# Performance work log

Measured on AMD Instinct MI355X. Metric: run time of the kernel, lower is better.

## Reference

```python
import jax, jax.numpy as jnp
import numpy as np

INF = 1e30  # sentinel for 'unreached' cost
MAX_ITERS = 512


def setup_inputs() -> dict:
    key = jax.random.key(0)
    img = jax.random.uniform(key, (3, 2048, 2048), dtype=jnp.float32)
    return {"img": img}


def _sobel_mag(gray):
    # gray: [H,W] -> gradient magnitude [H,W] (the 'processing_filter')
    kx = jnp.array([[-1.0, 0.0, 1.0], [-2.0, 0.0, 2.0], [-1.0, 0.0, 1.0]], gray.dtype)
    k = jnp.stack([kx, kx.T])[:, None]  # [2,1,3,3]
    g = jax.lax.conv_general_dilated(gray[None, None], k, (1, 1), 'SAME')[0]  # [2,H,W]
    return jnp.sqrt(g[0] ** 2 + g[1] ** 2)


def _neighbor_min(c):
    # min over 4-connected neighbors, INF padding at borders
    big_r = jnp.full((1, c.shape[1]), INF, c.dtype)
    big_c = jnp.full((c.shape[0], 1), INF, c.dtype)
    n = jnp.concatenate([big_r, c[:-1]], 0)
    s = jnp.concatenate([c[1:], big_r], 0)
    w = jnp.concatenate([big_c, c[:, :-1]], 1)
    e = jnp.concatenate([c[:, 1:], big_c], 1)
    return jnp.minimum(jnp.minimum(n, s), jnp.minimum(w, e))


def _relax(cost, img):
    # minimax-path (flood-level) relaxation: cost[p] = min(cost[p], max(min_nbr_cost, img[p]))
    return jnp.minimum(cost, jnp.maximum(_neighbor_min(cost), img))


def _watershed2(img, markers):
    # marker-based watershed on topography `img` with labels {1,2}.
    # Label of p = argmin over seed sets of the minimax path cost (flooding level),
    # which matches skimage.segmentation.watershed region assignment (4-connectivity).
    c1 = jnp.where(markers == 1, img, jnp.float32(INF))
    c2 = jnp.where(markers == 2, img, jnp.float32(INF))

    def cond(st):
        _, _, i, ch = st
        return jnp.logical_and(ch, i < MAX_ITERS)

    def body(st):
        c1, c2, i, _ = st
        n1 = _relax(c1, img)
        n2 = _relax(c2, img)
        ch = jnp.logical_or(jnp.any(n1 < c1), jnp.any(n2 < c2))
        return n1, n2, i + 1, ch

    c1, c2, _, _ = jax.lax.while_loop(cond, body, (c1, c2, jnp.int32(0), jnp.bool_(True)))
    return jnp.where(c2 < c1, jnp.float32(2.0), jnp.float32(1.0))


def _forward(img):
    gray = jnp.einsum('chw,c->hw', img, jnp.array([0.2989, 0.587, 0.114], img.dtype))
    filter_res = _sobel_mag(gray)  # [H,W]
    q_hi = jnp.quantile(filter_res, 0.9925)
    q_lo = jnp.quantile(filter_res, 0.9825)
    # torch sets 2 first, then 1, so pixels satisfying both end up as 1
    markers = jnp.where(filter_res <= q_lo, 1, jnp.where(filter_res >= q_hi, 2, 0))
    labels = _watershed2(gray, markers)[None]  # [1,H,W], values in {1,2}
    labels = labels - labels.min()
    return labels / labels.max()


def reference(img):
    return _forward(img)
```

## Files before the change

### kernel.cpp

```cpp
#include <hip/hip_runtime.h>
#include <hip/hip_cooperative_groups.h>

#define HH 2048
#define WW 2048
#define NPX (HH*WW)
#define INFV 1e30f
#define TS 128
#define NT 16
#define NTL 256
#define CY 32

namespace cg = cooperative_groups;

__device__ __forceinline__ void BARL(){
  __builtin_amdgcn_sched_barrier(0);
  asm volatile("s_waitcnt lgkmcnt(0)" ::: "memory");
  __builtin_amdgcn_s_barrier();
  __builtin_amdgcn_sched_barrier(0);
}

__device__ __forceinline__ float sobel_at(const float* __restrict__ g, int y, int x){
  float a00,a01,a02,a10,a12,a20,a21,a22;
  if (y>0 && y<HH-1 && x>0 && x<WW-1){
    const float* p = g + (size_t)(y-1)*WW + x;
    a00=p[-1]; a01=p[0]; a02=p[1];
    p += WW;   a10=p[-1];          a12=p[1];
    p += WW;   a20=p[-1]; a21=p[0]; a22=p[1];
  } else {
    auto at=[&](int yy,int xx)->float{
      return (yy<0||yy>=HH||xx<0||xx>=WW)?0.0f:g[(size_t)yy*WW+xx];
    };
    a00=at(y-1,x-1); a01=at(y-1,x); a02=at(y-1,x+1);
    a10=at(y,  x-1);                a12=at(y,  x+1);
    a20=at(y+1,x-1); a21=at(y+1,x); a22=at(y+1,x+1);
  }
  float gx = __fadd_rn(__fadd_rn(__fsub_rn(a02,a00), __fmul_rn(2.0f,__fsub_rn(a12,a10))), __fsub_rn(a22,a20));
  float gy = __fadd_rn(__fadd_rn(__fsub_rn(a20,a00), __fmul_rn(2.0f,__fsub_rn(a21,a01))), __fsub_rn(a22,a02));
  return sqrtf(__fadd_rn(__fmul_rn(gx,gx),__fmul_rn(gy,gy)));
}

__global__ void gray_kernel(const float* __restrict__ img, float* __restrict__ gray){
  const float* R=img; const float* G=img+NPX; const float* B=img+2*(size_t)NPX;
  for (int i=blockIdx.x*blockDim.x+threadIdx.x; i<NPX; i+=gridDim.x*blockDim.x){
    gray[i] = __fadd_rn(__fadd_rn(__fmul_rn(0.2989f,R[i]),__fmul_rn(0.587f,G[i])),__fmul_rn(0.114f,B[i]));
  }
}

__global__ void sobel_hist1(const float* __restrict__ gray, float* __restrict__ fr,
                            unsigned* __restrict__ hist){
  __shared__ unsigned h[4*2048];
  for (int i=threadIdx.x;i<4*2048;i+=blockDim.x) h[i]=0;
  __syncthreads();
  const int rep=(threadIdx.x&3)*2048;
  for (int i=blockIdx.x*blockDim.x+threadIdx.x; i<NPX; i+=gridDim.x*blockDim.x){
    int y=i>>11, x=i&(WW-1);
    float f=sobel_at(gray,y,x);
    fr[i]=f;
    unsigned key=__float_as_uint(f);
    atomicAdd(&h[rep+(key>>21)],1u);
  }
  __syncthreads();
  for (int i=threadIdx.x;i<2048;i+=blockDim.x){
    unsigned s=h[i]+h[i+2048]+h[i+4096]+h[i+6144];
    if (s) atomicAdd(&hist[i],s);
  }
}

__global__ void hist_l2(const float* __restrict__ fr, const unsigned* __restrict__ sel1,
                        unsigned* __restrict__ hist2){
  __shared__ unsigned h[4*2048];
  __shared__ unsigned sb[4];
  if (threadIdx.x<4) sb[threadIdx.x]=sel1[threadIdx.x];
  for (int i=threadIdx.x;i<4*2048;i+=blockDim.x) h[i]=0;
  __syncthreads();
  for (int i=blockIdx.x*blockDim.x+threadIdx.x; i<NPX; i+=gridDim.x*blockDim.x){
    unsigned key=__float_as_uint(fr[i]);
    unsigned b=key>>21, sub=(key>>10)&0x7FFu;
    #pragma unroll
    for (int k=0;k<4;++k) if (b==sb[k]) atomicAdd(&h[k*2048+sub],1u);
  }
  __syncthreads();
  for (int i=threadIdx.x;i<4*2048;i+=blockDim.x){ unsigned s=h[i]; if (s) atomicAdd(&hist2[i],s); }
}

__global__ void hist_l3(const float* __restrict__ fr, const unsigned* __restrict__ sel1,
                        const unsigned* __restrict__ sel2, unsigned* __restrict__ hist3){
  __shared__ unsigned h[4*1024];
  __shared__ unsigned pf[4];
  if (threadIdx.x<4) pf[threadIdx.x]=(sel1[threadIdx.x]<<11)|sel2[threadIdx.x];
  for (int i=threadIdx.x;i<4*1024;i+=blockDim.x) h[i]=0;
  __syncthreads();
  for (int i=blockIdx.x*blockDim.x+threadIdx.x; i<NPX; i+=gridDim.x*blockDim.x){
    unsigned key=__float_as_uint(fr[i]);
    unsigned p22=key>>10, sub=key&0x3FFu;
    #pragma unroll
    for (int k=0;k<4;++k) if (p22==pf[k]) atomicAdd(&h[k*1024+sub],1u);
  }
  __syncthreads();
  for (int i=threadIdx.x;i<4*1024;i+=blockDim.x){ unsigned s=h[i]; if (s) atomicAdd(&hist3[i],s); }
}

__global__ void scan_l1(const unsigned* __restrict__ hist, unsigned* __restrict__ sel1,
                        unsigned* __restrict__ rem1){
  __shared__ unsigned part[1024];
  const int t=threadIdx.x;
  unsigned a=hist[2*t], b=hist[2*t+1];
  part[t]=a+b; __syncthreads();
  for (int off=1;off<1024;off<<=1){
    unsigned add=(t>=off)?part[t-off]:0u; __syncthreads();
    part[t]+=add; __syncthreads();
  }
  unsigned before=(t>0)?part[t-1]:0u;
  const unsigned R[4]={4120902u,4120903u,4162845u,4162846u};
  unsigned cum=before;
  #pragma unroll
  for (int i=0;i<4;++i) if (R[i]>=cum && R[i]<cum+a){ sel1[i]=2*t;   rem1[i]=R[i]-cum; }
  cum+=a;
  #pragma unroll
  for (int i=0;i<4;++i) if (R[i]>=cum && R[i]<cum+b){ sel1[i]=2*t+1; rem1[i]=R[i]-cum; }
}

__global__ void scan_l2(const unsigned* __restrict__ hist2, const unsigned* __restrict__ rem1,
                        unsigned* __restrict__ sel2, unsigned* __restrict__ rem2){
  __shared__ unsigned part[1024];
  const int t=threadIdx.x;
  for (int i=0;i<4;++i){
    const unsigned* hh=hist2+i*2048;
    unsigned a=hh[2*t], b=hh[2*t+1];
    part[t]=a+b; __syncthreads();
    for (int off=1;off<1024;off<<=1){
      unsigned add=(t>=off)?part[t-off]:0u; __syncthreads();
      part[t]+=add; __syncthreads();
    }
    unsigned before=(t>0)?part[t-1]:0u;
    unsigned r=rem1[i], cum=before;
    if (r>=cum && r<cum+a){ sel2[i]=2*t;   rem2[i]=r-cum; }
    cum+=a;
    if (r>=cum && r<cum+b){ sel2[i]=2*t+1; rem2[i]=r-cum; }
    __syncthreads();
  }
}

__global__ void scan_l3(const unsigned* __restrict__ hist3, const unsigned* __restrict__ sel1,
                        const unsigned* __restrict__ sel2, const unsigned* __restrict__ rem2,
                        float* __restrict__ scal){
  __shared__ unsigned part[1024];
  __shared__ float vals[4];
  const int t=threadIdx.x;
  for (int i=0;i<4;++i){
    unsigned c=hist3[i*1024+t];
    part[t]=c; __syncthreads();
    for (int off=1;off<1024;off<<=1){
      unsigned add=(t>=off)?part[t-off]:0u; __syncthreads();
      part[t]+=add; __syncthreads();
    }
    unsigned before=(t>0)?part[t-1]:0u;
    unsigned r=rem2[i];
    if (r>=before && r<before+c){
      unsigned key=(sel1[i]<<21)|(sel2[i]<<10)|(unsigned)t;
      vals[i]=__uint_as_float(key);
    }
    __syncthreads();
  }
  if (t==0){
    scal[0]=__fadd_rn(__fmul_rn(vals[0],0.25f),__fmul_rn(vals[1],0.75f));
    scal[1]=__fadd_rn(__fmul_rn(vals[2],0.25f),__fmul_rn(vals[3],0.75f));
  }
}


#define HSCAN_LR(va,vb,gA,gB,hl) do{ \
  float ql_=gA[j], qh_=va[j]; \
  qh_=fminf(vb[j],fmaxf(gB[j],qh_)); ql_=fmaxf(gB[j],ql_); \
  _Pragma("unroll") \
  for (int d_=1;d_<64;d_<<=1){ \
    float pl_=__shfl_up(ql_,(unsigned)d_), ph_=__shfl_up(qh_,(unsigned)d_); \
    if (c>=d_){ qh_=fminf(qh_,fmaxf(ql_,ph_)); ql_=fmaxf(ql_,pl_); } \
  } \
  float E_=fminf(qh_,fmaxf(ql_,(hl))); \
  float In_=__shfl_up(E_,1u); if(c==0) In_=(hl); \
  float na_=fminf(va[j],fmaxf(gA[j],In_)); if(na_<va[j]){va[j]=na_;ch=true;} \
  float nb_=fminf(vb[j],fmaxf(gB[j],na_)); if(nb_<vb[j]){vb[j]=nb_;ch=true;} \
}while(0)

#define HSCAN_RL(va,vb,gA,gB,hr) do{ \
  float ql_=gB[j], qh_=vb[j]; \
  qh_=fminf(va[j],fmaxf(gA[j],qh_)); ql_=fmaxf(gA[j],ql_); \
  _Pragma("unroll") \
  for (int d_=1;d_<64;d_<<=1){ \
    float pl_=__shfl_down(ql_,(unsigned)d_), ph_=__shfl_down(qh_,(unsigned)d_); \
    if (c+d_<64){ qh_=fminf(qh_,fmaxf(ql_,ph_)); ql_=fmaxf(ql_,pl_); } \
  } \
  float E_=fminf(qh_,fmaxf(ql_,(hr))); \
  float In_=__shfl_down(E_,1u); if(c==63) In_=(hr); \
  float nb_=fminf(vb[j],fmaxf(gB[j],In_)); if(nb_<vb[j]){vb[j]=nb_;ch=true;} \
  float na_=fminf(va[j],fmaxf(gA[j],nb_)); if(na_<va[j]){va[j]=na_;ch=true;} \
}while(0)

#define VCOMP_DN(va,gA,Larr,Harr,XX) { float ql_=gA[0], qh_=va[0]; \
  _Pragma("unroll") for (int jj_=1;jj_<8;++jj_){ qh_=fminf(va[jj_],fmaxf(gA[jj_],qh_)); ql_=fmaxf(gA[jj_],ql_);} \
  Larr[w][XX]=ql_; Harr[w][XX]=qh_; }

#define VCOMP_UP(va,gA,Larr,Harr,XX) { float ql_=gA[7], qh_=va[7]; \
  _Pragma("unroll") for (int jj_=6;jj_>=0;--jj_){ qh_=fminf(va[jj_],fmaxf(gA[jj_],qh_)); ql_=fmaxf(gA[jj_],ql_);} \
  Larr[w][XX]=ql_; Harr[w][XX]=qh_; }

#define VAPPLY_DN(va,gA,Larr,XX) { float In_=Larr[w][XX]; \
  _Pragma("unroll") for (int jj_=0;jj_<8;++jj_){ float nv_=fminf(va[jj_],fmaxf(In_,gA[jj_])); if(nv_<va[jj_]){va[jj_]=nv_;ch=true;} In_=nv_; } }

#define VAPPLY_UP(va,gA,Larr,XX) { float In_=Larr[w][XX]; \
  _Pragma("unroll") for (int jj_=7;jj_>=0;--jj_){ float nv_=fminf(va[jj_],fmaxf(In_,gA[jj_])); if(nv_<va[jj_]){va[jj_]=nv_;ch=true;} In_=nv_; } }

#define CHAIN_DN(Harr,Larr,HT) { float E=HALO[HT][x]; \
  _Pragma("unroll") for (int b_=0;b_<16;++b_){ float I=E; E=fminf(Harr[b_][x],fmaxf(Larr[b_][x],I)); Larr[b_][x]=I; } }

#define CHAIN_UP(Harr,Larr,HB) { float E=HALO[HB][x]; \
  _Pragma("unroll") for (int b_=15;b_>=0;--b_){ float I=E; E=fminf(Harr[b_][x],fmaxf(Larr[b_][x],I)); Larr[b_][x]=I; } }

#define CHAINC_DN(Harr,Larr,Earr,HT,ECHV) { \
  float E=HALO[HT][x]; unsigned m_=0; \
  _Pragma("unroll") for (int b_=0;b_<16;++b_){ \
    float I_=E; E=fminf(Harr[b_][x],fmaxf(Larr[b_][x],I_)); \
    if (__any(I_!=Earr[b_][x])) m_|=(1u<<b_); \
    Earr[b_][x]=I_; } \
  if (c==0 && m_) atomicOr(&ECHV,(int)m_); }

#define CHAINC_UP(Harr,Larr,Earr,HB,ECHV) { \
  float E=HALO[HB][x]; unsigned m_=0; \
  _Pragma("unroll") for (int b_=15;b_>=0;--b_){ \
    float I_=E; E=fminf(Harr[b_][x],fmaxf(Larr[b_][x],I_)); \
    if (__any(I_!=Earr[b_][x])) m_|=(1u<<b_); \
    Earr[b_][x]=I_; } \
  if (c==0 && m_) atomicOr(&ECHV,(int)m_); }

#define HFIELD(va,vb,IHL,IHR) do{ \
  _Pragma("unroll") \
  for (int j=0;j<8;++j){ \
    const int r_=(w<<3)|j; \
    const float hl=HALO[IHL][r_], hr=HALO[IHR][r_]; \
    { float la_=__shfl_up(vb[j],1u); if(c==0) la_=hl; \
      bool p_=__any((fminf(va[j],fmaxf(la_,ga[j]))<va[j])||(fminf(vb[j],fmaxf(va[j],gb[j]))<vb[j])); \
      if (p_){ HSCAN_LR(va,vb,ga,gb,hl); } } \
    { float ra_=__shfl_down(va[j],1u); if(c==63) ra_=hr; \
      bool p_=__any((fminf(vb[j],fmaxf(ra_,gb[j]))<vb[j])||(fminf(va[j],fmaxf(vb[j],ga[j]))<va[j])); \
      if (p_){ HSCAN_RL(va,vb,ga,gb,hr); } } \
  } \
}while(0)

#define ASTORE(p,v) __hip_atomic_store((p),(v),__ATOMIC_RELAXED,__HIP_MEMORY_SCOPE_AGENT)
#define ALOAD(p)    __hip_atomic_load((p),__ATOMIC_RELAXED,__HIP_MEMORY_SCOPE_AGENT)

__global__ void __launch_bounds__(1024,4)
tile_solve(float* __restrict__ c1g, float* __restrict__ cg,
           const float* __restrict__ grayg, const float* __restrict__ scal)
{
  __shared__ float DNL1[16][128], DNH1[16][128], DNL2[16][128], DNH2[16][128];
  __shared__ float UPL1[16][128], UPH1[16][128], UPL2[16][128], UPH2[16][128];
  __shared__ float HALO[8][128];
  __shared__ int VN1[2],HN1[2],VN2[2],HN2[2];
  const int tid=threadIdx.x, w=tid>>6, c=tid&63;
  const int oty=blockIdx.x>>5, otx=blockIdx.x&31;
  const int wy0=oty*64-32, wx0=otx*64-32, x0=c<<1;
  const float qlo=scal[0], qhi=scal[1];
  HALO[tid>>7][tid&127]=INFV;
  if (tid==0){ VN1[0]=1;HN1[0]=1;VN2[0]=1;HN2[0]=1;
               VN1[1]=0;HN1[1]=0;VN2[1]=0;HN2[1]=0; }
  float v1a[8],v1b[8],v2a[8],v2b[8],ga[8],gb[8];
  const int gx=wx0+x0;
  #pragma unroll
  for (int j=0;j<8;++j){
    const int gy=wy0+(w<<3)+j;
    const bool rok=(gy>=0)&&(gy<HH);
    const bool aok=rok&&(gx>=0)&&(gx<WW), bok=rok&&(gx+1>=0)&&(gx+1<WW);
    float gA=INFV,gB=INFV,fA=0.0f,fB=0.0f;
    if (aok){ gA=grayg[(size_t)gy*WW+gx];   fA=sobel_at(grayg,gy,gx); }
    if (bok){ gB=grayg[(size_t)gy*WW+gx+1]; fB=sobel_at(grayg,gy,gx+1); }
    ga[j]=gA; gb[j]=gB;
    if (aok){ bool m1=(fA<=qlo); bool m2=(!m1)&&(fA>=qhi);
              v1a[j]=m1?gA:INFV; v2a[j]=(m1|m2)?gA:INFV; }
    else    { v1a[j]=INFV; v2a[j]=INFV; }
    if (bok){ bool m1=(fB<=qlo); bool m2=(!m1)&&(fB>=qhi);
              v1b[j]=m1?gB:INFV; v2b[j]=(m1|m2)?gB:INFV; }
    else    { v1b[j]=INFV; v2b[j]=INFV; }
  }
  __syncthreads();
  for (int cyc=0; cyc<24; ++cyc){
    const int cur=cyc&1, nxt=cur^1;
    const int vn1=VN1[cur], hn1=HN1[cur], vn2=VN2[cur], hn2=HN2[cur];
    if (!(vn1|hn1|vn2|hn2)) break;
    if (vn1){
      VCOMP_DN(v1a,ga,DNL1,DNH1,x0) VCOMP_DN(v1b,gb,DNL1,DNH1,x0+1)
      VCOMP_UP(v1a,ga,UPL1,UPH1,x0) VCOMP_UP(v1b,gb,UPL1,UPH1,x0+1)
    }
    if (vn2){
      VCOMP_DN(v2a,ga,DNL2,DNH2,x0) VCOMP_DN(v2b,gb,DNL2,DNH2,x0+1)
      VCOMP_UP(v2a,ga,UPL2,UPH2,x0) VCOMP_UP(v2b,gb,UPL2,UPH2,x0+1)
    }
    __syncthreads();
    if (w<8){
      const int x=((w&1)<<6)|c;
      const bool go=(w>>2)?(vn2!=0):(vn1!=0);
      if (go){
        switch(w>>1){
          case 0: CHAIN_DN(DNH1,DNL1,0) break;
          case 1: CHAIN_UP(UPH1,UPL1,2) break;
          case 2: CHAIN_DN(DNH2,DNL2,1) break;
          default:CHAIN_UP(UPH2,UPL2,3) break;
        }
      }
    }
    __syncthreads();
    if (vn1){ bool ch=false;
      VAPPLY_DN(v1a,ga,DNL1,x0) VAPPLY_DN(v1b,gb,DNL1,x0+1)
      VAPPLY_UP(v1a,ga,UPL1,x0) VAPPLY_UP(v1b,gb,UPL1,x0+1)
      if (ch) HN1[nxt]=1;
    }
    if (hn1){ bool ch=false;
      HFIELD(v1a,v1b,4,6);
      if (ch) VN1[nxt]=1;
    }
    if (vn2){ bool ch=false;
      VAPPLY_DN(v2a,ga,DNL2,x0) VAPPLY_DN(v2b,gb,DNL2,x0+1)
      VAPPLY_UP(v2a,ga,UPL2,x0) VAPPLY_UP(v2b,gb,UPL2,x0+1)
      if (ch) HN2[nxt]=1;
    }
    if (hn2){ bool ch=false;
      HFIELD(v2a,v2b,5,7);
      if (ch) VN2[nxt]=1;
    }
    if (tid==0){ VN1[cur]=0; HN1[cur]=0; VN2[cur]=0; HN2[cur]=0; }
    __syncthreads();
  }
  if (w>=4 && w<12 && c>=16 && c<48){
    #pragma unroll
    for (int j=0;j<8;++j){
      const int gy=wy0+(w<<3)+j;
      const size_t b=(size_t)gy*WW+gx;
      float2 o1; o1.x=v1a[j]; o1.y=v1b[j];
      float2 o2; o2.x=v2a[j]; o2.y=v2b[j];
      *(float2*)(c1g+b)=o1;
      *(float2*)(cg +b)=o2;
    }
  }
}

#define CYCLE(HV,CUR,NXT) do{ \
  if (hsrc){ \
    if (HV < HALO[harr][hx]){ \
      HALO[harr][hx]=HV; \
      if (harr<4){ if (harr&1) VN2[NXT]=1; else VN1[NXT]=1; } \
      else       { if (harr&1) HN2[NXT]=1; else HN1[NXT]=1; } \
    } \
    HV=ALOAD(hsrc); \
  } \
  const int vn1=VN1[CUR], hn1=HN1[CUR], vn2=VN2[CUR], hn2=HN2[CUR]; \
  const unsigned vd1=(unsigned)VD1s, vd2=(unsigned)VD2s; \
  if (!(vn1|hn1|vn2|hn2|(int)(vd1|vd2))){ \
    BARL(); \
  } else { \
     \
    if ((vd1>>w)&1){ \
      VCOMP_DN(v1a,ga,DNL1,DNH1,x0) VCOMP_DN(v1b,gb,DNL1,DNH1,x0+1) \
      VCOMP_UP(v1a,ga,UPL1,UPH1,x0) VCOMP_UP(v1b,gb,UPL1,UPH1,x0+1) \
    } \
    if ((vd2>>w)&1){ \
      VCOMP_DN(v2a,ga,DNL2,DNH2,x0) VCOMP_DN(v2b,gb,DNL2,DNH2,x0+1) \
      VCOMP_UP(v2a,ga,UPL2,UPH2,x0) VCOMP_UP(v2b,gb,UPL2,UPH2,x0+1) \
    } \
    if (tid==0){ ECH1s=0; ECH2s=0; } \
    BARL(); \
     \
    if (w<8){ \
      const int x=((w&1)<<6)|c; \
      switch(w>>1){ \
        case 0: if (vn1|(int)vd1) CHAINC_DN(DNH1,DNL1,EDN1,0,ECH1s) break; \
        case 1: if (vn1|(int)vd1) CHAINC_UP(UPH1,UPL1,EUP1,2,ECH1s) break; \
        case 2: if (vn2|(int)vd2) CHAINC_DN(DNH2,DNL2,EDN2,1,ECH2s) break; \
        default:if (vn2|(int)vd2) CHAINC_UP(UPH2,UPL2,EUP2,3,ECH2s) break; \
      } \
    } \
    if (tid==0){ VD1s=0; VD2s=0; } \
    BARL(); \
     \
    const unsigned am1=((unsigned)ECH1s)|vd1, am2=((unsigned)ECH2s)|vd2; \
    bool pf1=false, pf2=false; \
    { bool ch=false; \
      if ((am1>>w)&1){ \
        VAPPLY_DN(v1a,ga,EDN1,x0) VAPPLY_DN(v1b,gb,EDN1,x0+1) \
        VAPPLY_UP(v1a,ga,EUP1,x0) VAPPLY_UP(v1b,gb,EUP1,x0+1) \
      } \
      bool vch=__any(ch); \
      ch=false; \
      if (hn1){ HFIELD(v1a,v1b,4,6); } \
      bool hch=__any(ch); \
      if ((vch|hch) && c==0) atomicOr(&VD1s,1<<w); \
      if (vch) HN1[NXT]=1; \
      pf1 = vch|hch; \
    } \
    { bool ch=false; \
      if ((am2>>w)&1){ \
        VAPPLY_DN(v2a,ga,EDN2,x0) VAPPLY_DN(v2b,gb,EDN2,x0+1) \
        VAPPLY_UP(v2a,ga,EUP2,x0) VAPPLY_UP(v2b,gb,EUP2,x0+1) \
      } \
      bool vch=__any(ch); \
      ch=false; \
      if (hn2){ HFIELD(v2a,v2b,5,7); } \
      bool hch=__any(ch); \
      if ((vch|hch) && c==0) atomicOr(&VD2s,1<<w); \
      if (vch) HN2[NXT]=1; \
      pf2 = vch|hch; \
    } \
    if (pf1|pf2){ \
      if (w==0){ const int eb=(tile*4+0)*128; \
        if(pf1){ ASTORE(EB1+eb+x0,v1a[0]); ASTORE(EB1+eb+x0+1,v1b[0]); } \
        if(pf2){ ASTORE(EB2+eb+x0,v2a[0]); ASTORE(EB2+eb+x0+1,v2b[0]); } } \
      if (w==15){ const int eb=(tile*4+1)*128; \
        if(pf1){ ASTORE(EB1+eb+x0,v1a[7]); ASTORE(EB1+eb+x0+1,v1b[7]); } \
        if(pf2){ ASTORE(EB2+eb+x0,v2a[7]); ASTORE(EB2+eb+x0+1,v2b[7]); } } \
      if (c==0){ const int eb=(tile*4+2)*128+(w<<3); \
        _Pragma("unroll") \
        for (int j=0;j<8;++j){ if(pf1)ASTORE(EB1+eb+j,v1a[j]); if(pf2)ASTORE(EB2+eb+j,v2a[j]); } } \
      if (c==63){ const int eb=(tile*4+3)*128+(w<<3); \
        _Pragma("unroll") \
        for (int j=0;j<8;++j){ if(pf1)ASTORE(EB1+eb+j,v1b[j]); if(pf2)ASTORE(EB2+eb+j,v2b[j]); } } \
      if (c==1) wflag=1; \
    } \
    if (tid==0){ VN1[CUR]=0; HN1[CUR]=0; VN2[CUR]=0; HN2[CUR]=0; } \
    BARL(); \
  } \
}while(0)

__global__ void __launch_bounds__(1024,4)
ws_solve(float* __restrict__ c1g, const float* __restrict__ grayg, float* outg,
         int* __restrict__ flagIt)
{
  __shared__ float DNL1[16][128], DNH1[16][128], DNL2[16][128], DNH2[16][128];
  __shared__ float UPL1[16][128], UPH1[16][128], UPL2[16][128], UPH2[16][128];
  __shared__ float EDN1[16][128], EUP1[16][128], EDN2[16][128], EUP2[16][128];
  __shared__ float HALO[8][128];
  __shared__ int VN1[2],HN1[2],VN2[2],HN2[2];
  __shared__ int VD1s, VD2s, ECH1s, ECH2s;
  __shared__ int wflag;
  cg::grid_group grid = cg::this_grid();
  const int tid=threadIdx.x, w=tid>>6, c=tid&63;
  const int xcd=blockIdx.x&7, idx=blockIdx.x>>3;
  const int tx=((xcd&3)<<2)|(idx&3), ty=((xcd>>2)<<3)|(idx>>2);
  const int tile=ty*NT+tx;
  const int by=ty*TS, bx=tx*TS, x0=c<<1;
  float* EB1=outg;
  float* EB2=outg+(NTL*4*128);

  const int hx=tid&127, harr=tid>>7;
  const float* hsrc=nullptr;
  {
    const float* EB=(harr&1)?EB2:EB1;
    switch(harr>>1){
      case 0: if (ty>0)    hsrc=EB+((tile-NT)*4+1)*128+hx; break;
      case 1: if (ty<NT-1) hsrc=EB+((tile+NT)*4+0)*128+hx; break;
      case 2: if (tx>0)    hsrc=EB+((tile-1)*4+3)*128+hx;  break;
      default:if (tx<NT-1) hsrc=EB+((tile+1)*4+2)*128+hx;  break;
    }
  }

  float v1a[8],v1b[8],v2a[8],v2b[8],ga[8],gb[8];
  {
    size_t base=(size_t)(by+(w<<3))*WW + bx + x0;
    #pragma unroll
    for (int j=0;j<8;++j){
      float2 t1=*(const float2*)(c1g+base);
      float2 t2=*(const float2*)(outg+base);
      float2 tg=*(const float2*)(grayg+base);
      v1a[j]=t1.x; v1b[j]=t1.y; v2a[j]=t2.x; v2b[j]=t2.y; ga[j]=tg.x; gb[j]=tg.y;
      base+=(size_t)WW;
    }
  }
  grid.sync();

  if (w==0){ const int eb=(tile*4+0)*128;
    ASTORE(EB1+eb+x0,v1a[0]); ASTORE(EB1+eb+x0+1,v1b[0]);
    ASTORE(EB2+eb+x0,v2a[0]); ASTORE(EB2+eb+x0+1,v2b[0]); }
  if (w==15){ const int eb=(tile*4+1)*128;
    ASTORE(EB1+eb+x0,v1a[7]); ASTORE(EB1+eb+x0+1,v1b[7]);
    ASTORE(EB2+eb+x0,v2a[7]); ASTORE(EB2+eb+x0+1,v2b[7]); }
  if (c==0){ const int eb=(tile*4+2)*128+(w<<3);
    #pragma unroll
    for (int j=0;j<8;++j){ ASTORE(EB1+eb+j,v1a[j]); ASTORE(EB2+eb+j,v2a[j]); } }
  if (c==63){ const int eb=(tile*4+3)*128+(w<<3);
    #pragma unroll
    for (int j=0;j<8;++j){ ASTORE(EB1+eb+j,v1b[j]); ASTORE(EB2+eb+j,v2b[j]); } }
  HALO[harr][hx]=INFV;
  if (tid==0){ VN1[0]=1;HN1[0]=1;VN2[0]=1;HN2[0]=1;
               VN1[1]=0;HN1[1]=0;VN2[1]=0;HN2[1]=0;
               VD1s=0xFFFF; VD2s=0xFFFF; ECH1s=0; ECH2s=0; wflag=0; }
  __threadfence();
  grid.sync();

  float hvA=INFV, hvB=INFV;
  if (hsrc){ hvA=ALOAD(hsrc); hvB=ALOAD(hsrc); }

  for (int win=0; win<96; ++win){
    for (int cyc=0; cyc<CY; cyc+=2){
      CYCLE(hvA,0,1);
      CYCLE(hvB,1,0);
    }
    if (tid==0 && (wflag || (VD1s|VD2s))) atomicMax(flagIt,win+1);
    __threadfence();
    grid.sync();
    int fv=ALOAD(flagIt);
    if (fv<=win) break;
    if (tid==0) wflag=0;
    __syncthreads();
  }
  {
    size_t base=(size_t)(by+(w<<3))*WW + bx + x0;
    #pragma unroll
    for (int j=0;j<8;++j){
      float2 o; o.x=(v2a[j]<v1a[j])?1.0f:0.0f; o.y=(v2b[j]<v1b[j])?1.0f:0.0f;
      *(float2*)(outg+base)=o;
      base+=(size_t)WW;
    }
  }
}

extern "C" void kernel_launch(void* const* d_in, const int* in_sizes, int n_in,
                              void* d_out, int out_size, void* d_ws, size_t ws_size,
                              hipStream_t stream)
{
  const float* img=(const float*)d_in[0];
  float* out=(float*)d_out;
  char* wsb=(char*)d_ws;
  float* gray=(float*)wsb;
  float* c1  =(float*)(wsb + (size_t)NPX*4);
  unsigned* meta=(unsigned*)(wsb + (size_t)NPX*8);
  float* c2 = out;

  unsigned* hist1=meta;
  unsigned* hist2=meta+2048;
  unsigned* hist3=meta+10240;
  unsigned* sel1 =meta+14336;
  unsigned* rem1 =meta+14340;
  unsigned* sel2 =meta+14344;
  unsigned* rem2 =meta+14348;
  float*    scal =(float*)(meta+14352);
  int*      flagIt=(int*)(meta+14354);

  hipMemsetAsync(meta, 0, 14355*sizeof(unsigned), stream);
  hipLaunchKernelGGL(gray_kernel, dim3(4096), dim3(256), 0, stream, img, gray);
  hipLaunchKernelGGL(sobel_hist1, dim3(1024), dim3(256), 0, stream, gray, c1, hist1);
  hipLaunchKernelGGL(scan_l1, dim3(1), dim3(1024), 0, stream, hist1, sel1, rem1);
  hipLaunchKernelGGL(hist_l2, dim3(1024), dim3(256), 0, stream, c1, sel1, hist2);
  hipLaunchKernelGGL(scan_l2, dim3(1), dim3(1024), 0, stream, hist2, rem1, sel2, rem2);
  hipLaunchKernelGGL(hist_l3, dim3(1024), dim3(256), 0, stream, c1, sel1, sel2, hist3);
  hipLaunchKernelGGL(scan_l3, dim3(1), dim3(1024), 0, stream, hist3, sel1, sel2, rem2, scal);

  hipLaunchKernelGGL(tile_solve, dim3(1024), dim3(1024), 0, stream, c1, c2, gray, scal);

  void* args[]={ (void*)&c1,(void*)&gray,(void*)&out,(void*)&flagIt };
  (void)hipLaunchCooperativeKernel(ws_solve, dim3(NTL), dim3(1024), args, 0, stream);
}
```

Baseline: 597.0 us.

## Fuse grayscale into Sobel pass and restructure watershed cycle barriers

Merges the grayscale conversion kernel into the Sobel/histogram kernel, which recomputes gray from the RGB image at all nine stencil taps instead of reading a precomputed gray buffer. In the cooperative watershed solve, the per-cycle vertical compose step moves to the end of the previous cycle, so one block barrier per cycle goes away. Shared-memory atomicOr dirty masks are replaced with per-wave flag arrays written directly. The local tile_solve pre-pass cycle cap rises from 24 to 64, which trades more local iterations for fewer global windows. The fused Sobel pass does extra loads and arithmetic per pixel.

```diff
diff --git a/kernel.cpp b/kernel.cpp
--- a/kernel.cpp
+++ b/kernel.cpp
@@ -17,6 +17,13 @@
   asm volatile("s_waitcnt lgkmcnt(0)" ::: "memory");
   __builtin_amdgcn_s_barrier();
   __builtin_amdgcn_sched_barrier(0);
+}
+
+__device__ __forceinline__ float gray_at(const float* __restrict__ img, int y, int x){
+  if ((unsigned)y>=(unsigned)HH || (unsigned)x>=(unsigned)WW) return 0.0f;
+  const size_t i=(size_t)y*WW+x;
+  return __fadd_rn(__fadd_rn(__fmul_rn(0.2989f,img[i]),__fmul_rn(0.587f,img[i+(size_t)NPX])),
+                   __fmul_rn(0.114f,img[i+2*(size_t)NPX]));
 }
 
 __device__ __forceinline__ float sobel_at(const float* __restrict__ g, int y, int x){
@@ -39,22 +46,21 @@
   return sqrtf(__fadd_rn(__fmul_rn(gx,gx),__fmul_rn(gy,gy)));
 }
 
-__global__ void gray_kernel(const float* __restrict__ img, float* __restrict__ gray){
-  const float* R=img; const float* G=img+NPX; const float* B=img+2*(size_t)NPX;
-  for (int i=blockIdx.x*blockDim.x+threadIdx.x; i<NPX; i+=gridDim.x*blockDim.x){
-    gray[i] = __fadd_rn(__fadd_rn(__fmul_rn(0.2989f,R[i]),__fmul_rn(0.587f,G[i])),__fmul_rn(0.114f,B[i]));
-  }
-}
-
-__global__ void sobel_hist1(const float* __restrict__ gray, float* __restrict__ fr,
-                            unsigned* __restrict__ hist){
+__global__ void sobel_gray_hist1(const float* __restrict__ img, float* __restrict__ gray,
+                                 float* __restrict__ fr, unsigned* __restrict__ hist){
   __shared__ unsigned h[4*2048];
   for (int i=threadIdx.x;i<4*2048;i+=blockDim.x) h[i]=0;
   __syncthreads();
   const int rep=(threadIdx.x&3)*2048;
   for (int i=blockIdx.x*blockDim.x+threadIdx.x; i<NPX; i+=gridDim.x*blockDim.x){
     int y=i>>11, x=i&(WW-1);
-    float f=sobel_at(gray,y,x);
+    float a00=gray_at(img,y-1,x-1), a01=gray_at(img,y-1,x), a02=gray_at(img,y-1,x+1);
+    float a10=gray_at(img,y,  x-1), a11=gray_at(img,y,  x), a12=gray_at(img,y,  x+1);
+    float a20=gray_at(img,y+1,x-1), a21=gray_at(img,y+1,x), a22=gray_at(img,y+1,x+1);
+    gray[i]=a11;
+    float gx = __fadd_rn(__fadd_rn(__fsub_rn(a02,a00), __fmul_rn(2.0f,__fsub_rn(a12,a10))), __fsub_rn(a22,a20));
+    float gy = __fadd_rn(__fadd_rn(__fsub_rn(a20,a00), __fmul_rn(2.0f,__fsub_rn(a21,a01))), __fsub_rn(a22,a02));
+    float f = sqrtf(__fadd_rn(__fmul_rn(gx,gx),__fmul_rn(gy,gy)));
     fr[i]=f;
     unsigned key=__float_as_uint(f);
     atomicAdd(&h[rep+(key>>21)],1u);
@@ -217,21 +223,21 @@
 #define CHAIN_UP(Harr,Larr,HB) { float E=HALO[HB][x]; \
   _Pragma("unroll") for (int b_=15;b_>=0;--b_){ float I=E; E=fminf(Harr[b_][x],fmaxf(Larr[b_][x],I)); Larr[b_][x]=I; } }
 
-#define CHAINC_DN(Harr,Larr,Earr,HT,ECHV) { \
+#define CHAINCM_DN(Harr,Larr,Earr,HT,DST) { \
   float E=HALO[HT][x]; unsigned m_=0; \
   _Pragma("unroll") for (int b_=0;b_<16;++b_){ \
     float I_=E; E=fminf(Harr[b_][x],fmaxf(Larr[b_][x],I_)); \
     if (__any(I_!=Earr[b_][x])) m_|=(1u<<b_); \
     Earr[b_][x]=I_; } \
-  if (c==0 && m_) atomicOr(&ECHV,(int)m_); }
-
-#define CHAINC_UP(Harr,Larr,Earr,HB,ECHV) { \
+  if (c==0) DST=(int)m_; }
+
+#define CHAINCM_UP(Harr,Larr,Earr,HB,DST) { \
   float E=HALO[HB][x]; unsigned m_=0; \
   _Pragma("unroll") for (int b_=15;b_>=0;--b_){ \
     float I_=E; E=fminf(Harr[b_][x],fmaxf(Larr[b_][x],I_)); \
     if (__any(I_!=Earr[b_][x])) m_|=(1u<<b_); \
     Earr[b_][x]=I_; } \
-  if (c==0 && m_) atomicOr(&ECHV,(int)m_); }
+  if (c==0) DST=(int)m_; }
 
 #define HFIELD(va,vb,IHL,IHR) do{ \
   _Pragma("unroll") \
@@ -284,7 +290,7 @@
     else    { v1b[j]=INFV; v2b[j]=INFV; }
   }
   __syncthreads();
-  for (int cyc=0; cyc<24; ++cyc){
+  for (int cyc=0; cyc<64; ++cyc){
     const int cur=cyc&1, nxt=cur^1;
     const int vn1=VN1[cur], hn1=HN1[cur], vn2=VN2[cur], hn2=HN2[cur];
     if (!(vn1|hn1|vn2|hn2)) break;
@@ -354,61 +360,60 @@
     HV=ALOAD(hsrc); \
   } \
   const int vn1=VN1[CUR], hn1=HN1[CUR], vn2=VN2[CUR], hn2=HN2[CUR]; \
-  const unsigned vd1=(unsigned)VD1s, vd2=(unsigned)VD2s; \
-  if (!(vn1|hn1|vn2|hn2|(int)(vd1|vd2))){ \
+  const int vda1=VDA1[CUR], vda2=VDA2[CUR]; \
+  const int myvd1=VDB1[CUR][w], myvd2=VDB2[CUR][w]; \
+  if (!(vn1|hn1|vn2|hn2|vda1|vda2)){ \
     BARL(); \
   } else { \
-     \
-    if ((vd1>>w)&1){ \
-      VCOMP_DN(v1a,ga,DNL1,DNH1,x0) VCOMP_DN(v1b,gb,DNL1,DNH1,x0+1) \
-      VCOMP_UP(v1a,ga,UPL1,UPH1,x0) VCOMP_UP(v1b,gb,UPL1,UPH1,x0+1) \
-    } \
-    if ((vd2>>w)&1){ \
-      VCOMP_DN(v2a,ga,DNL2,DNH2,x0) VCOMP_DN(v2b,gb,DNL2,DNH2,x0+1) \
-      VCOMP_UP(v2a,ga,UPL2,UPH2,x0) VCOMP_UP(v2b,gb,UPL2,UPH2,x0+1) \
-    } \
-    if (tid==0){ ECH1s=0; ECH2s=0; } \
-    BARL(); \
-     \
+    const int chv1=vn1|vda1, chv2=vn2|vda2; \
     if (w<8){ \
       const int x=((w&1)<<6)|c; \
       switch(w>>1){ \
-        case 0: if (vn1|(int)vd1) CHAINC_DN(DNH1,DNL1,EDN1,0,ECH1s) break; \
-        case 1: if (vn1|(int)vd1) CHAINC_UP(UPH1,UPL1,EUP1,2,ECH1s) break; \
-        case 2: if (vn2|(int)vd2) CHAINC_DN(DNH2,DNL2,EDN2,1,ECH2s) break; \
-        default:if (vn2|(int)vd2) CHAINC_UP(UPH2,UPL2,EUP2,3,ECH2s) break; \
+        case 0: if (chv1) CHAINCM_DN(DNH1,DNL1,EDN1,0,ECHDN1[w&1]) break; \
+        case 1: if (chv1) CHAINCM_UP(UPH1,UPL1,EUP1,2,ECHUP1[w&1]) break; \
+        case 2: if (chv2) CHAINCM_DN(DNH2,DNL2,EDN2,1,ECHDN2[w&1]) break; \
+        default:if (chv2) CHAINCM_UP(UPH2,UPL2,EUP2,3,ECHUP2[w&1]) break; \
       } \
     } \
-    if (tid==0){ VD1s=0; VD2s=0; } \
     BARL(); \
-     \
-    const unsigned am1=((unsigned)ECH1s)|vd1, am2=((unsigned)ECH2s)|vd2; \
+    const unsigned em1 = chv1 ? (unsigned)(ECHDN1[0]|ECHDN1[1]|ECHUP1[0]|ECHUP1[1]) : 0u; \
+    const unsigned em2 = chv2 ? (unsigned)(ECHDN2[0]|ECHDN2[1]|ECHUP2[0]|ECHUP2[1]) : 0u; \
     bool pf1=false, pf2=false; \
     { bool ch=false; \
-      if ((am1>>w)&1){ \
+      if (((em1>>w)&1)|myvd1){ \
         VAPPLY_DN(v1a,ga,EDN1,x0) VAPPLY_DN(v1b,gb,EDN1,x0+1) \
         VAPPLY_UP(v1a,ga,EUP1,x0) VAPPLY_UP(v1b,gb,EUP1,x0+1) \
       } \
-      bool vch=__any(ch); \
-      ch=false; \
+      bool vch=__any(ch); ch=false; \
       if (hn1){ HFIELD(v1a,v1b,4,6); } \
       bool hch=__any(ch); \
-      if ((vch|hch) && c==0) atomicOr(&VD1s,1<<w); \
+      bool chg=vch|hch; \
+      if (chg){ \
+        VCOMP_DN(v1a,ga,DNL1,DNH1,x0) VCOMP_DN(v1b,gb,DNL1,DNH1,x0+1) \
+        VCOMP_UP(v1a,ga,UPL1,UPH1,x0) VCOMP_UP(v1b,gb,UPL1,UPH1,x0+1) \
+        VDA1[NXT]=1; \
+      } \
+      if (c==0) VDB1[NXT][w]=chg?1:0; \
       if (vch) HN1[NXT]=1; \
-      pf1 = vch|hch; \
+      pf1=chg; \
     } \
     { bool ch=false; \
-      if ((am2>>w)&1){ \
+      if (((em2>>w)&1)|myvd2){ \
         VAPPLY_DN(v2a,ga,EDN2,x0) VAPPLY_DN(v2b,gb,EDN2,x0+1) \
         VAPPLY_UP(v2a,ga,EUP2,x0) VAPPLY_UP(v2b,gb,EUP2,x0+1) \
       } \
-      bool vch=__any(ch); \
-      ch=false; \
+      bool vch=__any(ch); ch=false; \
       if (hn2){ HFIELD(v2a,v2b,5,7); } \
       bool hch=__any(ch); \
-      if ((vch|hch) && c==0) atomicOr(&VD2s,1<<w); \
+      bool chg=vch|hch; \
+      if (chg){ \
+        VCOMP_DN(v2a,ga,DNL2,DNH2,x0) VCOMP_DN(v2b,gb,DNL2,DNH2,x0+1) \
+        VCOMP_UP(v2a,ga,UPL2,UPH2,x0) VCOMP_UP(v2b,gb,UPL2,UPH2,x0+1) \
+        VDA2[NXT]=1; \
+      } \
+      if (c==0) VDB2[NXT][w]=chg?1:0; \
       if (vch) HN2[NXT]=1; \
-      pf2 = vch|hch; \
+      pf2=chg; \
     } \
     if (pf1|pf2){ \
       if (w==0){ const int eb=(tile*4+0)*128; \
@@ -425,7 +430,8 @@
         for (int j=0;j<8;++j){ if(pf1)ASTORE(EB1+eb+j,v1b[j]); if(pf2)ASTORE(EB2+eb+j,v2b[j]); } } \
       if (c==1) wflag=1; \
     } \
-    if (tid==0){ VN1[CUR]=0; HN1[CUR]=0; VN2[CUR]=0; HN2[CUR]=0; } \
+    if (tid==0){ VN1[CUR]=0; HN1[CUR]=0; VN2[CUR]=0; HN2[CUR]=0; \
+                 VDA1[CUR]=0; VDA2[CUR]=0; } \
     BARL(); \
   } \
 }while(0)
@@ -439,7 +445,9 @@
   __shared__ float EDN1[16][128], EUP1[16][128], EDN2[16][128], EUP2[16][128];
   __shared__ float HALO[8][128];
   __shared__ int VN1[2],HN1[2],VN2[2],HN2[2];
-  __shared__ int VD1s, VD2s, ECH1s, ECH2s;
+  __shared__ int VDB1[2][16], VDB2[2][16];
+  __shared__ int VDA1[2], VDA2[2];
+  __shared__ int ECHDN1[2],ECHUP1[2],ECHDN2[2],ECHUP2[2];
   __shared__ int wflag;
   cg::grid_group grid = cg::this_grid();
   const int tid=threadIdx.x, w=tid>>6, c=tid&63;
@@ -491,7 +499,14 @@
   HALO[harr][hx]=INFV;
   if (tid==0){ VN1[0]=1;HN1[0]=1;VN2[0]=1;HN2[0]=1;
                VN1[1]=0;HN1[1]=0;VN2[1]=0;HN2[1]=0;
-               VD1s=0xFFFF; VD2s=0xFFFF; ECH1s=0; ECH2s=0; wflag=0; }
+               VDA1[0]=1;VDA2[0]=1;VDA1[1]=0;VDA2[1]=0; wflag=0;
+               ECHDN1[0]=0;ECHDN1[1]=0;ECHUP1[0]=0;ECHUP1[1]=0;
+               ECHDN2[0]=0;ECHDN2[1]=0;ECHUP2[0]=0;ECHUP2[1]=0; }
+  if (tid<16){ VDB1[0][tid]=1; VDB2[0][tid]=1; VDB1[1][tid]=0; VDB2[1][tid]=0; }
+  VCOMP_DN(v1a,ga,DNL1,DNH1,x0) VCOMP_DN(v1b,gb,DNL1,DNH1,x0+1)
+  VCOMP_UP(v1a,ga,UPL1,UPH1,x0) VCOMP_UP(v1b,gb,UPL1,UPH1,x0+1)
+  VCOMP_DN(v2a,ga,DNL2,DNH2,x0) VCOMP_DN(v2b,gb,DNL2,DNH2,x0+1)
+  VCOMP_UP(v2a,ga,UPL2,UPH2,x0) VCOMP_UP(v2b,gb,UPL2,UPH2,x0+1)
   __threadfence();
   grid.sync();
 
@@ -503,7 +518,7 @@
       CYCLE(hvA,0,1);
       CYCLE(hvB,1,0);
     }
-    if (tid==0 && (wflag || (VD1s|VD2s))) atomicMax(flagIt,win+1);
+    if (tid==0 && (wflag || VDA1[0]|VDA1[1]|VDA2[0]|VDA2[1])) atomicMax(flagIt,win+1);
     __threadfence();
     grid.sync();
     int fv=ALOAD(flagIt);
@@ -545,8 +560,7 @@
   int*      flagIt=(int*)(meta+14354);
 
   hipMemsetAsync(meta, 0, 14355*sizeof(unsigned), stream);
-  hipLaunchKernelGGL(gray_kernel, dim3(4096), dim3(256), 0, stream, img, gray);
-  hipLaunchKernelGGL(sobel_hist1, dim3(1024), dim3(256), 0, stream, gray, c1, hist1);
+  hipLaunchKernelGGL(sobel_gray_hist1, dim3(1024), dim3(256), 0, stream, img, gray, c1, hist1);
   hipLaunchKernelGGL(scan_l1, dim3(1), dim3(1024), 0, stream, hist1, sel1, rem1);
   hipLaunchKernelGGL(hist_l2, dim3(1024), dim3(256), 0, stream, c1, sel1, hist2);
   hipLaunchKernelGGL(scan_l2, dim3(1), dim3(1024), 0, stream, hist2, rem1, sel2, rem2);
```

New measurement: 622.3 us. 4.2% more time.
